# Optimization experiments

Measured on AMD Instinct MI355X. Metric: run time of the kernel, lower is better.

The kernel has to match this reference:

```python
import jax, jax.numpy as jnp
import numpy as np

# Dimensions
O, D, F_LSOA = 128, 128, 64      # origins, destinations, LSOA feature dim
T, FE, H = 128, 16, 64           # max seq len, edge_feature_dim, gru_hidden
NH, NO, PH = 128, 64, 128        # node_hidden, node_out, pair_hidden
P = O * D                        # number of O-D pairs


def _mlp3(x, W1, b1, W2, b2, W3, b3):
    # Linear->ReLU->Linear->ReLU->Linear (dropout is identity in eval mode)
    h = jax.nn.relu(x @ W1 + b1)
    h = jax.nn.relu(h @ W2 + b2)
    return h @ W3 + b3


def setup_inputs() -> dict:
    key = jax.random.key(0)
    ks = jax.random.split(key, 32)

    def rn(k, shape, s):
        return jax.random.normal(k, shape, dtype=jnp.float32) * s

    inp = {
        "O_feats": rn(ks[0], (O, F_LSOA), 1.0),
        "D_feats": rn(ks[1], (D, F_LSOA), 1.0),
        "seqs": rn(ks[2], (P, T, FE), 1.0),
        "lengths": jax.random.randint(ks[3], (P,), 1, T + 1, dtype=jnp.int32),
        # enc_O
        "WO1": rn(ks[4], (F_LSOA, NH), 0.05), "bO1": jnp.zeros((NH,), jnp.float32),
        "WO2": rn(ks[5], (NH, NH), 0.05),     "bO2": jnp.zeros((NH,), jnp.float32),
        "WO3": rn(ks[6], (NH, NO), 0.05),     "bO3": jnp.zeros((NO,), jnp.float32),
        # enc_D
        "WD1": rn(ks[7], (F_LSOA, NH), 0.05), "bD1": jnp.zeros((NH,), jnp.float32),
        "WD2": rn(ks[8], (NH, NH), 0.05),     "bD2": jnp.zeros((NH,), jnp.float32),
        "WD3": rn(ks[9], (NH, NO), 0.05),     "bD3": jnp.zeros((NO,), jnp.float32),
        # pair_head: 2*node_out -> pair_hidden -> 1
        "Wp1": rn(ks[10], (2 * NO, PH), 0.05), "bp1": jnp.zeros((PH,), jnp.float32),
        "Wp2": rn(ks[11], (PH, 1), 0.05),      "bp2": jnp.zeros((1,), jnp.float32),
        # GRU (gate order r, z, n as in PyTorch)
        "W_ih": rn(ks[12], (FE, 3 * H), 0.1),  "b_ih": jnp.zeros((3 * H,), jnp.float32),
        "W_hh": rn(ks[13], (H, 3 * H), 0.1),   "b_hh": jnp.zeros((3 * H,), jnp.float32),
        # seq_head
        "Ws": rn(ks[14], (H, 1), 0.1),         "bs": jnp.zeros((1,), jnp.float32),
    }
    return inp


def reference(O_feats, D_feats, seqs, lengths,
              WO1, bO1, WO2, bO2, WO3, bO3,
              WD1, bD1, WD2, bD2, WD3, bD3,
              Wp1, bp1, Wp2, bp2,
              W_ih, W_hh, b_ih, b_hh,
              Ws, bs):
    # Node encoders
    eo = _mlp3(O_feats, WO1, bO1, WO2, bO2, WO3, bO3)   # [O, NO]
    ed = _mlp3(D_feats, WD1, bD1, WD2, bD2, WD3, bD3)   # [D, NO]

    # Pairwise score: concat(eo, ed) -> MLP -> softplus
    pair_in = jnp.concatenate([
        jnp.broadcast_to(eo[:, None, :], (O, D, NO)),
        jnp.broadcast_to(ed[None, :, :], (O, D, NO)),
    ], axis=-1)                                          # [O, D, 2*NO]
    hp = jax.nn.relu(pair_in @ Wp1 + bp1)                # [O, D, PH]
    z_pair = (hp @ Wp2 + bp2)[..., 0]                    # [O, D]
    s_pair = jax.nn.softplus(z_pair)

    # Length-masked GRU over all O*D padded sequences (equiv. to pack_padded)
    xT = jnp.swapaxes(seqs, 0, 1)                        # [T, P, FE]
    h0 = jnp.zeros((P, H), jnp.float32)

    def step(h, inp):
        xt, t = inp
        gx = xt @ W_ih + b_ih                            # [P, 3H]
        gh = h @ W_hh + b_hh                             # [P, 3H]
        xr, xz, xn = jnp.split(gx, 3, axis=-1)
        hr, hz, hn = jnp.split(gh, 3, axis=-1)
        r = jax.nn.sigmoid(xr + hr)
        zg = jax.nn.sigmoid(xz + hz)
        n = jnp.tanh(xn + r * hn)
        h_new = (1.0 - zg) * n + zg * h
        h = jnp.where((t < lengths)[:, None], h_new, h)  # freeze past seq end
        return h, None

    h_last, _ = jax.lax.scan(step, h0, (xT, jnp.arange(T)))  # [P, H]

    p_seq = jax.nn.sigmoid(h_last @ Ws + bs)[:, 0].reshape(O, D)
    return jnp.sum(s_pair * p_seq)
```

## Files before the change

### kernel.cpp

```cpp
#include <hip/hip_runtime.h>
#include <hip/hip_bf16.h>

#define O_N 128
#define D_N 128
#define F_LS 64
#define T_MAX 128
#define FE_N 16
#define H_GRU 64
#define NH 128
#define NO 64
#define PH 128

typedef _Float16 f16;
typedef __fp16 hf2 __attribute__((ext_vector_type(2)));
typedef f16 f16x4 __attribute__((ext_vector_type(4)));
typedef f16 f16x8 __attribute__((ext_vector_type(8)));
typedef float f32x4 __attribute__((ext_vector_type(4)));

__device__ __forceinline__ float fast_sigmoid(float x) {
    return __builtin_amdgcn_rcpf(1.f + __expf(-x));
}

__global__ __launch_bounds__(128) void k_enc(
    const float* __restrict__ O_feats, const float* __restrict__ D_feats,
    const float* __restrict__ WO1, const float* __restrict__ bO1,
    const float* __restrict__ WO2, const float* __restrict__ bO2,
    const float* __restrict__ WO3, const float* __restrict__ bO3,
    const float* __restrict__ WD1, const float* __restrict__ bD1,
    const float* __restrict__ WD2, const float* __restrict__ bD2,
    const float* __restrict__ WD3, const float* __restrict__ bD3,
    const float* __restrict__ Wp1, const float* __restrict__ bp1,
    float* __restrict__ PA, float* __restrict__ PBt, float* __restrict__ d_out)
{
    __shared__ float h1[NH];
    __shared__ float h2[NH];
    __shared__ float ev[NO];
    const int b = blockIdx.x;
    const int enc = b >> 7;
    const int row = b & 127;
    const int t = threadIdx.x;
    if (b == 0 && t == 0) d_out[0] = 0.f;

    const float* x  = (enc ? D_feats : O_feats) + row * F_LS;
    const float* W1 = enc ? WD1 : WO1;  const float* b1 = enc ? bD1 : bO1;
    const float* W2 = enc ? WD2 : WO2;  const float* b2 = enc ? bD2 : bO2;
    const float* W3 = enc ? WD3 : WO3;  const float* b3 = enc ? bD3 : bO3;

    float a = b1[t];
    #pragma unroll 8
    for (int k = 0; k < F_LS; ++k) a += x[k] * W1[k * NH + t];
    h1[t] = fmaxf(a, 0.f);
    __syncthreads();

    a = b2[t];
    #pragma unroll 8
    for (int k = 0; k < NH; ++k) a += h1[k] * W2[k * NH + t];
    h2[t] = fmaxf(a, 0.f);
    __syncthreads();

    if (t < NO) {
        a = b3[t];
        #pragma unroll 8
        for (int k = 0; k < NH; ++k) a += h2[k] * W3[k * NO + t];
        ev[t] = a;
    }
    __syncthreads();

    const float* Wp = Wp1 + (enc ? NO * PH : 0);
    a = 0.f;
    #pragma unroll 8
    for (int k = 0; k < NO; ++k) a += ev[k] * Wp[k * PH + t];
    if (enc) PBt[t * 128 + row] = a + bp1[t];
    else     PA[row * PH + t] = a;
}

__global__ __launch_bounds__(128) void k_pair(
    const float* __restrict__ PA, const float* __restrict__ PBt,
    const float* __restrict__ Wp2, const float* __restrict__ bp2,
    float* __restrict__ s_pair)
{
    const int i = blockIdx.x;
    const int j = threadIdx.x;
    __shared__ float pa[PH];
    __shared__ float w2s[PH];
    pa[j]  = PA[i * PH + j];
    w2s[j] = Wp2[j];
    __syncthreads();
    float acc = 0.f;
    #pragma unroll 8
    for (int c = 0; c < PH; ++c)
        acc += w2s[c] * fmaxf(pa[c] + PBt[c * 128 + j], 0.f);
    float z = acc + bp2[0];
    float sp = fmaxf(z, 0.f) + log1pf(__expf(-fabsf(z)));
    s_pair[i * 128 + j] = sp;
}

__global__ __launch_bounds__(1024) void k_sort(
    const int* __restrict__ lengths, int* __restrict__ perm)
{
    __shared__ int cnt[130];
    __shared__ int suf[130];
    const int t = threadIdx.x;
    if (t < 130) cnt[t] = 0;
    __syncthreads();
    for (int i = t; i < 16384; i += 1024) atomicAdd(&cnt[lengths[i]], 1);
    __syncthreads();
    if (t < 130) suf[t] = cnt[t];
    __syncthreads();
    for (int d = 1; d < 130; d <<= 1) {
        int v = 0;
        if (t < 130) { v = suf[t]; if (t + d < 130) v += suf[t + d]; }
        __syncthreads();
        if (t < 130) suf[t] = v;
        __syncthreads();
    }
    if (t < 129) cnt[t] = (t + 1 < 130) ? suf[t + 1] : 0;
    __syncthreads();
    for (int i = t; i < 16384; i += 1024) {
        int pos = atomicAdd(&cnt[lengths[i]], 1);
        perm[pos] = i;
    }
}

__global__ __launch_bounds__(256, 4) void k_gru(
    const float* __restrict__ seqs, const int* __restrict__ lengths,
    const int* __restrict__ perm,
    const float* __restrict__ W_ih, const float* __restrict__ b_ih,
    const float* __restrict__ W_hh, const float* __restrict__ b_hh,
    const float* __restrict__ Ws, const float* __restrict__ bs,
    const float* __restrict__ s_pair, float* __restrict__ d_out)
{
    __shared__ __align__(16) f16 hbuf[2][16 * 72];
    __shared__ float red[64];
    const int tid = threadIdx.x;
    const int w  = tid >> 6;
    const int l  = tid & 63;
    const int q  = l >> 4;
    const int n  = l & 15;
    const int c  = w * 16 + n;
    const int colbase = w * 16 + q * 4;
    const int g  = (blockIdx.x & 255) * 4 + (blockIdx.x >> 8);
    const int pb = g * 16;
    const float S_RZ = -1.4426950408889634f;
    const float S_N  =  2.8853900817779268f;

    f16x8 wh[3][2], wi[3];
    #pragma unroll
    for (int gg = 0; gg < 3; ++gg) {
        const int gb = gg * 64;
        const float s = (gg < 2) ? S_RZ : S_N;
        #pragma unroll
        for (int ks = 0; ks < 2; ++ks)
            #pragma unroll
            for (int j = 0; j < 8; ++j)
                wh[gg][ks][j] = (f16)(W_hh[(ks * 32 + q * 8 + j) * 192 + gb + c] * s);
        #pragma unroll
        for (int j = 0; j < 8; ++j) {
            int k = q * 8 + j;
            wi[gg][j] = (k < FE_N) ? (f16)(W_ih[k * 192 + gb + c] * s) : (f16)0.f;
        }
    }
    f32x4 c_r, c_z, c_hn, c_xn;
    float wsc[4];
    #pragma unroll
    for (int r = 0; r < 4; ++r) {
        int col = colbase + r;
        c_r[r]  = S_RZ * (b_ih[col] + b_hh[col]);
        c_z[r]  = S_RZ * (b_ih[64 + col] + b_hh[64 + col]);
        c_hn[r] = S_N * b_hh[128 + col];
        c_xn[r] = S_N * b_ih[128 + col];
        wsc[r]  = Ws[col];
    }
    const int myp   = perm[pb + n];
    const int mylen = lengths[myp];
    int ml = mylen;
    ml = max(ml, __shfl_xor(ml, 1));
    ml = max(ml, __shfl_xor(ml, 2));
    ml = max(ml, __shfl_xor(ml, 4));
    ml = max(ml, __shfl_xor(ml, 8));
    const int maxlen = __builtin_amdgcn_readfirstlane(ml);

    {
        f16x8 z8 = {};
        if (tid < 144) *(f16x8*)&hbuf[0][tid * 8] = z8;
    }

    const float4* xp = (const float4*)(seqs + (size_t)myp * (T_MAX * FE_N)) + q * 2;
    float4 x0a = {0.f, 0.f, 0.f, 0.f}, x0b = x0a, x1a = x0a, x1b = x0a;
    if (q < 2) {
        x0a = xp[0]; x0b = xp[1];
        x1a = xp[4]; x1b = xp[5];
    }
    f16x8 ax = {};
    float hold[4] = {0.f, 0.f, 0.f, 0.f};
    __syncthreads();

    auto step = [&](int TT, int sub, float4& XA, float4& XB) {
        const f16* hb  = hbuf[sub];
        f16*       hbw = hbuf[sub ^ 1];
        f16x8 bh0 = *(const f16x8*)&hb[n * 72 + 8 * q];
        f16x8 bh1 = *(const f16x8*)&hb[n * 72 + 32 + 8 * q];
        if (q < 2) {
            union { f16x8 v8; hf2 v2[4]; } u;
            u.v2[0] = __builtin_amdgcn_cvt_pkrtz(XA.x, XA.y);
            u.v2[1] = __builtin_amdgcn_cvt_pkrtz(XA.z, XA.w);
            u.v2[2] = __builtin_amdgcn_cvt_pkrtz(XB.x, XB.y);
            u.v2[3] = __builtin_amdgcn_cvt_pkrtz(XB.z, XB.w);
            ax = u.v8;
            int tn = (TT + 2 < maxlen) ? (TT + 2) : (maxlen - 1);
            XA = xp[tn * 4]; XB = xp[tn * 4 + 1];
        }
        f32x4 ar = __builtin_amdgcn_mfma_f32_16x16x32_f16(wi[0], ax, c_r, 0, 0, 0);
        f32x4 az = __builtin_amdgcn_mfma_f32_16x16x32_f16(wi[1], ax, c_z, 0, 0, 0);
        f32x4 xn = __builtin_amdgcn_mfma_f32_16x16x32_f16(wi[2], ax, c_xn, 0, 0, 0);
        ar = __builtin_amdgcn_mfma_f32_16x16x32_f16(wh[0][0], bh0, ar, 0, 0, 0);
        ar = __builtin_amdgcn_mfma_f32_16x16x32_f16(wh[0][1], bh1, ar, 0, 0, 0);
        az = __builtin_amdgcn_mfma_f32_16x16x32_f16(wh[1][0], bh0, az, 0, 0, 0);
        az = __builtin_amdgcn_mfma_f32_16x16x32_f16(wh[1][1], bh1, az, 0, 0, 0);
        f32x4 hn = __builtin_amdgcn_mfma_f32_16x16x32_f16(wh[2][0], bh0, c_hn, 0, 0, 0);
        hn = __builtin_amdgcn_mfma_f32_16x16x32_f16(wh[2][1], bh1, hn, 0, 0, 0);

        const bool live = (TT < mylen);
        #pragma unroll
        for (int r = 0; r < 4; ++r) {
            float rg    = __builtin_amdgcn_rcpf(1.f + __builtin_amdgcn_exp2f(ar[r]));
            float zg    = __builtin_amdgcn_rcpf(1.f + __builtin_amdgcn_exp2f(az[r]));
            float inner = fmaf(rg, hn[r], xn[r]);
            float nn    = fmaf(-2.f, __builtin_amdgcn_rcpf(1.f + __builtin_amdgcn_exp2f(inner)), 1.f);
            float hnew  = fmaf(zg, hold[r] - nn, nn);
            hold[r] = live ? hnew : hold[r];
        }
        union { f16x4 v4; hf2 v2[2]; } hu;
        hu.v2[0] = __builtin_amdgcn_cvt_pkrtz(hold[0], hold[1]);
        hu.v2[1] = __builtin_amdgcn_cvt_pkrtz(hold[2], hold[3]);
        *(f16x4*)&hbw[n * 72 + colbase] = hu.v4;
    };

    #pragma unroll 1
    for (int t = 0; t < maxlen; t += 2) {
        step(t, 0, x0a, x0b);
        __syncthreads();
        if (t + 1 >= maxlen) break;
        step(t + 1, 1, x1a, x1b);
        __syncthreads();
    }

    float part = hold[0] * wsc[0] + hold[1] * wsc[1] +
                 hold[2] * wsc[2] + hold[3] * wsc[3];
    part += __shfl_xor(part, 16);
    part += __shfl_xor(part, 32);
    if (l < 16) red[w * 16 + n] = part;
    __syncthreads();
    if (tid < 16) {
        float s = red[tid] + red[16 + tid] + red[32 + tid] + red[48 + tid];
        float pv = fast_sigmoid(s + bs[0]);
        float contrib = s_pair[perm[pb + tid]] * pv;
        #pragma unroll
        for (int off = 1; off < 16; off <<= 1)
            contrib += __shfl_xor(contrib, off);
        if (tid == 0) atomicAdd(d_out, contrib);
    }
}

extern "C" void kernel_launch(void* const* d_in, const int* in_sizes, int n_in,
                              void* d_out, int out_size, void* d_ws, size_t ws_size,
                              hipStream_t stream)
{
    const float* O_feats = (const float*)d_in[0];
    const float* D_feats = (const float*)d_in[1];
    const float* seqs    = (const float*)d_in[2];
    const int*   lengths = (const int*)d_in[3];
    const float* WO1 = (const float*)d_in[4];  const float* bO1 = (const float*)d_in[5];
    const float* WO2 = (const float*)d_in[6];  const float* bO2 = (const float*)d_in[7];
    const float* WO3 = (const float*)d_in[8];  const float* bO3 = (const float*)d_in[9];
    const float* WD1 = (const float*)d_in[10]; const float* bD1 = (const float*)d_in[11];
    const float* WD2 = (const float*)d_in[12]; const float* bD2 = (const float*)d_in[13];
    const float* WD3 = (const float*)d_in[14]; const float* bD3 = (const float*)d_in[15];
    const float* Wp1 = (const float*)d_in[16]; const float* bp1 = (const float*)d_in[17];
    const float* Wp2 = (const float*)d_in[18]; const float* bp2 = (const float*)d_in[19];
    const float* W_ih = (const float*)d_in[20]; const float* b_ih = (const float*)d_in[21];
    const float* W_hh = (const float*)d_in[22]; const float* b_hh = (const float*)d_in[23];
    const float* Ws   = (const float*)d_in[24]; const float* bs   = (const float*)d_in[25];

    float* out    = (float*)d_out;
    float* PA     = (float*)d_ws;
    float* PBt    = PA + 128 * 128;
    float* s_pair = PBt + 128 * 128;
    int*   perm   = (int*)(s_pair + 16384);

    k_enc<<<256, 128, 0, stream>>>(O_feats, D_feats,
                                   WO1, bO1, WO2, bO2, WO3, bO3,
                                   WD1, bD1, WD2, bD2, WD3, bD3,
                                   Wp1, bp1, PA, PBt, out);
    k_pair<<<128, 128, 0, stream>>>(PA, PBt, Wp2, bp2, s_pair);
    k_sort<<<1, 1024, 0, stream>>>(lengths, perm);
    k_gru<<<1024, 256, 0, stream>>>(seqs, lengths, perm, W_ih, b_ih, W_hh, b_hh,
                                    Ws, bs, s_pair, out);
}
```

Measured before the change: 384.4 us.

## Stage GRU input timesteps into LDS with async global_load_lds double buffering

Each block now fetches its 16 sequences' input features eight timesteps at a time straight from global memory into a double-buffered LDS tile with global_load_lds. Each step then reads its input from LDS instead of from register prefetches issued two steps ahead. This is meant to take global-load latency and register pressure off the serial recurrence. The change also drops the interleaved block-to-group mapping in favour of a plain linear one, which may hurt load balance across CUs because the groups are sorted by length. The two-step manual unroll is folded into a single loop.

```diff
diff --git a/kernel.cpp b/kernel.cpp
--- a/kernel.cpp
+++ b/kernel.cpp
@@ -131,6 +131,7 @@
     const float* __restrict__ s_pair, float* __restrict__ d_out)
 {
     __shared__ __align__(16) f16 hbuf[2][16 * 72];
+    __shared__ __align__(16) float xbuf[2][8][16][16];
     __shared__ float red[64];
     const int tid = threadIdx.x;
     const int w  = tid >> 6;
@@ -139,8 +140,7 @@
     const int n  = l & 15;
     const int c  = w * 16 + n;
     const int colbase = w * 16 + q * 4;
-    const int g  = (blockIdx.x & 255) * 4 + (blockIdx.x >> 8);
-    const int pb = g * 16;
+    const int pb = blockIdx.x * 16;
     const float S_RZ = -1.4426950408889634f;
     const float S_N  =  2.8853900817779268f;
 
@@ -180,36 +180,58 @@
     ml = max(ml, __shfl_xor(ml, 8));
     const int maxlen = __builtin_amdgcn_readfirstlane(ml);
 
-    {
-        f16x8 z8 = {};
-        if (tid < 144) *(f16x8*)&hbuf[0][tid * 8] = z8;
-    }
-
-    const float4* xp = (const float4*)(seqs + (size_t)myp * (T_MAX * FE_N)) + q * 2;
-    float4 x0a = {0.f, 0.f, 0.f, 0.f}, x0b = x0a, x1a = x0a, x1b = x0a;
-    if (q < 2) {
-        x0a = xp[0]; x0b = xp[1];
-        x1a = xp[4]; x1b = xp[5];
-    }
-    f16x8 ax = {};
+    const float* xsrc = seqs + (size_t)perm[pb + (l >> 2)] * (T_MAX * FE_N)
+                       + (l & 3) * 4;
+
+    if (tid < 144) { f16x8 z8 = {}; *(f16x8*)&hbuf[0][tid * 8] = z8; }
+
+    #pragma unroll
+    for (int rr = 0; rr < 2; ++rr) {
+        const int r8 = w + rr * 4;
+        __builtin_amdgcn_global_load_lds(
+            (const __attribute__((address_space(1))) void*)(xsrc + (size_t)r8 * FE_N),
+            (__attribute__((address_space(3))) void*)&xbuf[0][r8][0][0], 16, 0, 0);
+    }
     float hold[4] = {0.f, 0.f, 0.f, 0.f};
-    __syncthreads();
-
-    auto step = [&](int TT, int sub, float4& XA, float4& XB) {
-        const f16* hb  = hbuf[sub];
-        f16*       hbw = hbuf[sub ^ 1];
+    const f16x8 zero8 = {};
+    __syncthreads();
+
+    #pragma unroll 1
+    for (int t = 0; t < maxlen; ++t) {
+        const int cur = t & 1;
+        const int xb  = (t >> 3) & 1;
+        const int row = t & 7;
+        const f16* hb  = hbuf[cur];
+        f16*       hbw = hbuf[cur ^ 1];
         f16x8 bh0 = *(const f16x8*)&hb[n * 72 + 8 * q];
         f16x8 bh1 = *(const f16x8*)&hb[n * 72 + 32 + 8 * q];
+
+        if (row == 0 && t + 8 < maxlen) {
+            const int nb = xb ^ 1;
+            #pragma unroll
+            for (int rr = 0; rr < 2; ++rr) {
+                const int rl = w + rr * 4;
+                int rg = t + 8 + rl;
+                rg = rg < T_MAX ? rg : T_MAX - 1;
+                __builtin_amdgcn_global_load_lds(
+                    (const __attribute__((address_space(1))) void*)(xsrc + (size_t)rg * FE_N),
+                    (__attribute__((address_space(3))) void*)&xbuf[nb][rl][0][0], 16, 0, 0);
+            }
+        }
+
+        f16x8 ax = zero8;
         if (q < 2) {
+            const float* xr = &xbuf[xb][row][n][q * 8];
+            float4 a0 = *(const float4*)xr;
+            float4 a1 = *(const float4*)(xr + 4);
             union { f16x8 v8; hf2 v2[4]; } u;
-            u.v2[0] = __builtin_amdgcn_cvt_pkrtz(XA.x, XA.y);
-            u.v2[1] = __builtin_amdgcn_cvt_pkrtz(XA.z, XA.w);
-            u.v2[2] = __builtin_amdgcn_cvt_pkrtz(XB.x, XB.y);
-            u.v2[3] = __builtin_amdgcn_cvt_pkrtz(XB.z, XB.w);
+            u.v2[0] = __builtin_amdgcn_cvt_pkrtz(a0.x, a0.y);
+            u.v2[1] = __builtin_amdgcn_cvt_pkrtz(a0.z, a0.w);
+            u.v2[2] = __builtin_amdgcn_cvt_pkrtz(a1.x, a1.y);
+            u.v2[3] = __builtin_amdgcn_cvt_pkrtz(a1.z, a1.w);
             ax = u.v8;
-            int tn = (TT + 2 < maxlen) ? (TT + 2) : (maxlen - 1);
-            XA = xp[tn * 4]; XB = xp[tn * 4 + 1];
         }
+
         f32x4 ar = __builtin_amdgcn_mfma_f32_16x16x32_f16(wi[0], ax, c_r, 0, 0, 0);
         f32x4 az = __builtin_amdgcn_mfma_f32_16x16x32_f16(wi[1], ax, c_z, 0, 0, 0);
         f32x4 xn = __builtin_amdgcn_mfma_f32_16x16x32_f16(wi[2], ax, c_xn, 0, 0, 0);
@@ -220,7 +242,7 @@
         f32x4 hn = __builtin_amdgcn_mfma_f32_16x16x32_f16(wh[2][0], bh0, c_hn, 0, 0, 0);
         hn = __builtin_amdgcn_mfma_f32_16x16x32_f16(wh[2][1], bh1, hn, 0, 0, 0);
 
-        const bool live = (TT < mylen);
+        const bool live = (t < mylen);
         #pragma unroll
         for (int r = 0; r < 4; ++r) {
             float rg    = __builtin_amdgcn_rcpf(1.f + __builtin_amdgcn_exp2f(ar[r]));
@@ -234,14 +256,6 @@
         hu.v2[0] = __builtin_amdgcn_cvt_pkrtz(hold[0], hold[1]);
         hu.v2[1] = __builtin_amdgcn_cvt_pkrtz(hold[2], hold[3]);
         *(f16x4*)&hbw[n * 72 + colbase] = hu.v4;
-    };
-
-    #pragma unroll 1
-    for (int t = 0; t < maxlen; t += 2) {
-        step(t, 0, x0a, x0b);
-        __syncthreads();
-        if (t + 1 >= maxlen) break;
-        step(t + 1, 1, x1a, x1b);
         __syncthreads();
     }
 
```

After: 328.7 us. 14.5% less time.
